# Kernel optimization log

Hardware: AMD Instinct MI355X
Metric: run time of the kernel (lower is better)

The kernel has to match this reference:

```python
import jax, jax.numpy as jnp
import numpy as np

E, C, L, B = 8, 128, 1024, 32
FB = L // 2 + 1        # 513 freq bins
HD = 2 * FB            # 1026 hidden dim


def setup_inputs() -> dict:
    key = jax.random.key(0)
    ks = jax.random.split(key, 8)
    return {
        "X_time": jax.random.normal(ks[0], (B, C, L), jnp.float32),
        "bound_params": jax.random.normal(ks[1], (E - 1,), jnp.float32),
        "W1r": jax.random.normal(ks[2], (E, HD, FB), jnp.float32) * 0.1,
        "W1i": jax.random.normal(ks[3], (E, HD, FB), jnp.float32) * 0.1,
        "b1r": jnp.zeros((E, HD), jnp.float32),
        "b1i": jnp.zeros((E, HD), jnp.float32),
        "W2r": jax.random.normal(ks[4], (E, FB, HD), jnp.float32) * 0.1,
        "W2i": jax.random.normal(ks[5], (E, FB, HD), jnp.float32) * 0.1,
        "b2r": jnp.zeros((E, FB), jnp.float32),
        "b2i": jnp.zeros((E, FB), jnp.float32),
        "gate_W": jax.random.normal(ks[6], (E, FB), jnp.float32) * 0.1,
        "gate_b": jnp.zeros((E,), jnp.float32),
    }


def reference(X_time, bound_params, W1r, W1i, b1r, b1i, W2r, W2i, b2r, b2i, gate_W, gate_b):
    Bx, Cx, Lx = X_time.shape
    fb = Lx // 2 + 1
    e = W1r.shape[0]

    Xf = jnp.fft.rfft(X_time, axis=-1)                     # [B,C,FB] complex

    # learnable frequency-band binary masks
    raw = jax.nn.sigmoid(bound_params)
    bounds = jnp.sort(jnp.concatenate([jnp.zeros(1, raw.dtype), raw, jnp.ones(1, raw.dtype)]))
    idx = (bounds * (fb - 1)).astype(jnp.int32)
    starts = idx[:e]
    ends = jnp.concatenate([idx[1:e], jnp.array([fb], jnp.int32)])
    pos = jnp.arange(fb)
    masks = ((pos[None, :] >= starts[:, None]) & (pos[None, :] < ends[:, None])).astype(X_time.dtype)  # [E,FB]

    # masked spectra per expert, split into real/imag: [E,B,C,FB]
    m = masks[:, None, None, :]
    xr = Xf.real * m
    xi = Xf.imag * m

    # expert layer 1: complex linear (W [E,HD,FB]) + complex ReLU
    hr = jnp.einsum('ehf,ebcf->ebch', W1r, xr) - jnp.einsum('ehf,ebcf->ebch', W1i, xi) + b1r[:, None, None, :]
    hi = jnp.einsum('ehf,ebcf->ebch', W1r, xi) + jnp.einsum('ehf,ebcf->ebch', W1i, xr) + b1i[:, None, None, :]
    hr = jax.nn.relu(hr)
    hi = jax.nn.relu(hi)

    # expert layer 2: complex linear (W [E,FB,HD]) -> [E,B,C,FB]
    yr = jnp.einsum('efh,ebch->ebcf', W2r, hr) - jnp.einsum('efh,ebch->ebcf', W2i, hi) + b2r[:, None, None, :]
    yi = jnp.einsum('efh,ebch->ebcf', W2r, hi) + jnp.einsum('efh,ebch->ebcf', W2i, hr) + b2i[:, None, None, :]

    # gate: mean |Xf| over channels -> linear -> softmax over experts
    mag = jnp.mean(jnp.abs(Xf), axis=1)                    # [B,FB]
    gate = jax.nn.softmax(mag @ gate_W.T + gate_b, axis=-1)  # [B,E]

    comb_r = jnp.einsum('ebcf,be->bcf', yr, gate)
    comb_i = jnp.einsum('ebcf,be->bcf', yi, gate)
    return jnp.fft.irfft(jax.lax.complex(comb_r, comb_i), n=Lx, axis=-1)
```

## Files before the change

### kernel.cpp

```cpp
#include <hip/hip_runtime.h>
#include <hip/hip_bf16.h>
#include <math.h>

typedef __hip_bfloat16 bf16;
typedef __attribute__((ext_vector_type(8))) short short8;
typedef __attribute__((ext_vector_type(4))) float f32x4;

#define FB 513
#define HD 1026
#define NN 1024
#define MR 4096
#define NE 8
#define BATCH 32

#define XINT_LD 1280
#define BIAS_LD 1056
#define FINV_LD 1088
#define HP_LD   2080
#define B1_ROWS 2176
#define KCAT    16640
#define MAG_LD  520
#define FF_ROWS 1280

__device__ __forceinline__ void gload16(const void* g, void* l) {
    __builtin_amdgcn_global_load_lds((const __attribute__((address_space(1))) void*)g,
                                     (__attribute__((address_space(3))) void*)l, 16, 0, 0);
}
__device__ __forceinline__ bf16 f2b(float v) { return __float2bfloat16(v); }
__device__ __forceinline__ unsigned short f2bu(float v) {
    bf16 b = __float2bfloat16(v);
    return *reinterpret_cast<unsigned short*>(&b);
}
__device__ __forceinline__ float bu2f(unsigned short u) {
    return __uint_as_float(((unsigned)u) << 16);
}
__device__ __forceinline__ unsigned pack2(float a, float b) {
    return (unsigned)f2bu(a) | ((unsigned)f2bu(b) << 16);
}

__device__ __forceinline__ void xcd_swizzle(int* px, int* py) {
    int gx = gridDim.x;
    int orig = blockIdx.x + gx * blockIdx.y;
    int q = (gx * gridDim.y) >> 3;
    int wg = (orig & 7) * q + (orig >> 3);
    *px = wg % gx;
    *py = wg / gx;
}

__global__ void prep_kernel(const float* __restrict__ bp, int* __restrict__ se) {
    if (threadIdx.x == 0 && blockIdx.x == 0) {
        float b[9];
        b[0] = 0.0f; b[8] = 1.0f;
        for (int i = 0; i < 7; i++) b[i + 1] = 1.0f / (1.0f + expf(-bp[i]));
        for (int i = 1; i < 9; i++) { float v = b[i]; int j = i - 1;
            while (j >= 0 && b[j] > v) { b[j + 1] = b[j]; j--; } b[j + 1] = v; }
        int idx[9];
        for (int i = 0; i < 9; i++) idx[i] = (int)(b[i] * (float)(FB - 1));
        for (int e = 0; e < NE; e++) {
            se[2 * e] = idx[e];
            se[2 * e + 1] = (e < NE - 1) ? idx[e + 1] : FB;
        }
    }
}

#define N_FF  ((long)FF_ROWS * NN)
#define N_FI  (1024L * FINV_LD)
#define N_B1P ((long)NE * B1_ROWS * (XINT_LD / 2))
#define N_XP  ((long)MR * NN / 2)
#define N_PREP (N_FF + N_FI + N_B1P + N_XP)

__global__ void prep_bulk(const float* __restrict__ W1r, const float* __restrict__ W1i,
                          const float* __restrict__ X, const int* __restrict__ se,
                          bf16* __restrict__ Ffwd, bf16* __restrict__ Finv,
                          bf16* __restrict__ B1, bf16* __restrict__ Xb) {
    long i = (long)blockIdx.x * 256 + threadIdx.x;
    const float TWO_PI = 6.283185307179586f;
    if (i < N_FF) {
        int n = (int)(i >> 10), t = (int)(i & (NN - 1));
        float v = 0.0f;
        if (n < 2 * FB) {
            int f = n >> 1, k = (f * t) & (NN - 1);
            float s, c; sincosf(TWO_PI * (float)k / (float)NN, &s, &c);
            v = (n & 1) ? -s : c;
        }
        Ffwd[i] = f2b(v);
        return;
    }
    i -= N_FF;
    if (i < N_FI) {
        int t = (int)(i / FINV_LD), k = (int)(i % FINV_LD);
        float v = 0.0f;
        if (k < 2 * FB) {
            int f = k >> 1, kk = (f * t) & (NN - 1);
            float s, c; sincosf(TWO_PI * (float)kk / (float)NN, &s, &c);
            float cf = (f == 0 || f == FB - 1) ? 1.0f : 2.0f;
            float sc = cf * (1.0f / (float)NN);
            v = (k & 1) ? -s * sc : c * sc;
        }
        Finv[i] = f2b(v);
        return;
    }
    i -= N_FI;
    if (i < N_B1P) {
        int f = (int)(i % (XINT_LD / 2));
        long t = i / (XINT_LD / 2);
        int n = (int)(t % B1_ROWS);
        int e = (int)(t / B1_ROWS);
        float ve = 0.0f, vo = 0.0f;
        if (n < 2 * HD && f < FB && f >= se[2 * e] && f < se[2 * e + 1]) {
            int hi_part = (n >= HD);
            int h = hi_part ? n - HD : n;
            long wi = ((long)e * HD + h) * FB + f;
            float wr = W1r[wi], wim = W1i[wi];
            ve = hi_part ? wim : wr;
            vo = hi_part ? wr : -wim;
        }
        *(unsigned*)(B1 + ((size_t)(e * B1_ROWS + n)) * XINT_LD + 2 * f) = pack2(ve, vo);
        return;
    }
    i -= N_B1P;
    if (i < N_XP) {
        float2 v = ((const float2*)X)[i];
        *(unsigned*)(Xb + 2 * i) = pack2(v.x, v.y);
    }
}

__global__ void pack_B2t(const float* __restrict__ W2r, const float* __restrict__ W2i,
                         bf16* __restrict__ B2t) {
    __shared__ float sR[64][65], sI[64][65];
    int e = blockIdx.z;
    int f0 = blockIdx.x * 64;
    int h0 = blockIdx.y * 64;
    int tid = threadIdx.x;
#pragma unroll
    for (int rep = 0; rep < 16; rep++) {
        int idx = tid + rep * 256;
        int fl = idx >> 6, hl = idx & 63;
        int f = f0 + fl, h = h0 + hl;
        bool ok = (f < FB) && (h < HD);
        size_t wi = ((size_t)e * FB + f) * HD + h;
        sR[fl][hl] = ok ? W2r[wi] : 0.0f;
        sI[fl][hl] = ok ? W2i[wi] : 0.0f;
    }
    __syncthreads();
#pragma unroll
    for (int rep = 0; rep < 4; rep++) {
        int idx = tid + rep * 256;
        int hl = idx >> 4, ch = idx & 15;
        int h = h0 + hl;
        int c0 = 2 * f0 + ch * 8;
        if (c0 >= FINV_LD) continue;
        short8 lo, hi;
#pragma unroll
        for (int j = 0; j < 4; j++) {
            int fl = ch * 4 + j;
            float wr = sR[fl][hl], wim = sI[fl][hl];
            lo[2 * j]     = (short)f2bu(wr);
            lo[2 * j + 1] = (short)f2bu(wim);
            hi[2 * j]     = (short)f2bu(-wim);
            hi[2 * j + 1] = (short)f2bu(wr);
        }
        if (h < HD) {
            *(short8*)(B2t + ((size_t)e * HP_LD + h) * FINV_LD + c0) = lo;
            *(short8*)(B2t + ((size_t)e * HP_LD + HD + h) * FINV_LD + c0) = hi;
        } else if (HD + h < HP_LD) {
            short8 z = {};
            *(short8*)(B2t + ((size_t)e * HP_LD + HD + h) * FINV_LD + c0) = z;
        }
    }
}

__global__ void mag_kernel(const bf16* __restrict__ Xint, float* __restrict__ magp) {
    int b = blockIdx.x, g = blockIdx.y, t = threadIdx.x;
    float acc[3] = {0.0f, 0.0f, 0.0f};
    const bf16* base = Xint + ((size_t)b * 128 + g * 16) * XINT_LD;
    for (int c = 0; c < 16; c++) {
        const bf16* row = base + (size_t)c * XINT_LD;
#pragma unroll
        for (int kk = 0; kk < 3; kk++) {
            int f = t + 256 * kk;
            if (f < FB) {
                float xr = __bfloat162float(row[2 * f]);
                float xi = __bfloat162float(row[2 * f + 1]);
                acc[kk] += sqrtf(xr * xr + xi * xi);
            }
        }
    }
#pragma unroll
    for (int kk = 0; kk < 3; kk++) {
        int f = t + 256 * kk;
        if (f < FB) magp[((size_t)b * 8 + g) * MAG_LD + f] = acc[kk];
    }
}

__global__ void gate_bias_kernel(const float* __restrict__ magp, const float* __restrict__ gW,
                                 const float* __restrict__ gb, const float* __restrict__ b2r,
                                 const float* __restrict__ b2i, float* __restrict__ gate,
                                 float* __restrict__ biasCs) {
    __shared__ float sred[256];
    __shared__ float sg[8];
    int b = blockIdx.x, tid = threadIdx.x;
    int e = tid & 7, j = tid >> 3;
    float acc = 0.0f;
    for (int f = j; f < FB; f += 32) {
        float m = 0.0f;
#pragma unroll
        for (int g = 0; g < 8; g++) m += magp[((size_t)b * 8 + g) * MAG_LD + f];
        acc += m * (1.0f / 128.0f) * gW[e * FB + f];
    }
    sred[tid] = acc;
    __syncthreads();
    if (tid < 64) {
        float a = sred[tid] + sred[tid + 64] + sred[tid + 128] + sred[tid + 192];
        a += __shfl_xor(a, 8); a += __shfl_xor(a, 16); a += __shfl_xor(a, 32);
        float logit = a + gb[e];
        float mx = logit;
        mx = fmaxf(mx, __shfl_xor(mx, 1)); mx = fmaxf(mx, __shfl_xor(mx, 2)); mx = fmaxf(mx, __shfl_xor(mx, 4));
        float ex = expf(logit - mx);
        float sum = ex;
        sum += __shfl_xor(sum, 1); sum += __shfl_xor(sum, 2); sum += __shfl_xor(sum, 4);
        if (tid < 8) { float g_ = ex / sum; sg[tid] = g_; gate[b * NE + tid] = g_; }
    }
    __syncthreads();
    for (int c = tid; c < BIAS_LD; c += 256) {
        float v = 0.0f;
        if (c < 2 * FB) {
            int f = c >> 1;
            const float* bb = (c & 1) ? b2i : b2r;
#pragma unroll
            for (int ee = 0; ee < NE; ee++) v += sg[ee] * bb[ee * FB + f];
            float cf = (f == 0 || f == FB - 1) ? 1.0f : 2.0f;
            v *= cf * (1.0f / (float)NN);
        }
        biasCs[b * BIAS_LD + c] = v;
    }
}

__global__ void biasT_kernel(const float* __restrict__ biasCs, const bf16* __restrict__ Ffwd,
                             float* __restrict__ biasT) {
    int t = blockIdx.x * 256 + threadIdx.x;
    int b = blockIdx.y;
    float s = 0.0f;
    for (int c = 0; c < 2 * FB; c++)
        s += biasCs[b * BIAS_LD + c] * __bfloat162float(Ffwd[(size_t)c * NN + t]);
    biasT[b * NN + t] = s;
}

__global__ void reduce_out4(const bf16* __restrict__ planes, const float* __restrict__ biasT,
                            float* __restrict__ out) {
    long idx = (long)blockIdx.x * 256 + threadIdx.x;
    if (idx >= (long)MR * NN / 8) return;
    size_t base = (size_t)idx * 8;
    long r = base >> 10;
    int t = (int)(base & (NN - 1));
    float s[8] = {};
#pragma unroll
    for (int z = 0; z < 4; z++) {
        short8 v = *(const short8*)(planes + (size_t)z * MR * NN + base);
#pragma unroll
        for (int j = 0; j < 8; j++) s[j] += bu2f((unsigned short)v[j]);
    }
    const float* bT = biasT + (r >> 7) * NN + t;
    float4 o0 = {s[0] + bT[0], s[1] + bT[1], s[2] + bT[2], s[3] + bT[3]};
    float4 o1 = {s[4] + bT[4], s[5] + bT[5], s[6] + bT[6], s[7] + bT[7]};
    *(float4*)(out + base) = o0;
    *(float4*)(out + base + 4) = o1;
}

template <int EPI>
__global__ void gemm_mfma(const bf16* __restrict__ A, int lda,
                          const bf16* __restrict__ B, int ldb, size_t zBstride,
                          void* __restrict__ Cv, int ldc, size_t zCoff,
                          int N, int K, int kPerZ,
                          const int* __restrict__ se2,
                          const float* __restrict__ biasR, const float* __restrict__ biasI,
                          int zBias, const float* __restrict__ gate8) {
    __shared__ bf16 As[128 * 32];
    __shared__ bf16 Bs[128 * 32];
    int tid = threadIdx.x;
    int zz = blockIdx.z;
    int bx, by;
    xcd_swizzle(&bx, &by);
    int row0 = by * 128, col0 = bx * 128;
    const bf16* Bz = B + (size_t)zz * zBstride;

    int kS, kE;
    if (EPI == 1) { int s = se2[2 * zz], e = se2[2 * zz + 1]; kS = (2 * s) & ~31; kE = (2 * e + 31) & ~31; }
    else          { kS = zz * kPerZ; kE = min(K, kS + kPerZ); }

    f32x4 acc[4][4] = {};

    int lane = tid & 63, wid = tid >> 6;
    int wrB = (wid >> 1) << 6, wcB = (wid & 1) << 6;
    int lr = lane & 15, lk = (lane >> 4) << 3;

    int r_a = tid >> 2, c_a = (tid & 3) << 3;
    int r_b = (tid + 256) >> 2, c_b = ((tid + 256) & 3) << 3;

    for (int kt = kS; kt < kE; kt += 32) {
        gload16(A + (size_t)(row0 + r_a) * lda + kt + c_a, &As[(size_t)tid * 8]);
        gload16(A + (size_t)(row0 + r_b) * lda + kt + c_b, &As[((size_t)tid + 256) * 8]);
        gload16(Bz + (size_t)(col0 + r_a) * ldb + kt + c_a, &Bs[(size_t)tid * 8]);
        gload16(Bz + (size_t)(col0 + r_b) * ldb + kt + c_b, &Bs[((size_t)tid + 256) * 8]);
        __syncthreads();
        short8 av[4], bv[4];
#pragma unroll
        for (int m = 0; m < 4; m++)
            av[m] = *(const short8*)&As[(wrB + m * 16 + lr) * 32 + lk];
#pragma unroll
        for (int n = 0; n < 4; n++)
            bv[n] = *(const short8*)&Bs[(wcB + n * 16 + lr) * 32 + lk];
#pragma unroll
        for (int m = 0; m < 4; m++)
#pragma unroll
            for (int n = 0; n < 4; n++)
                acc[m][n] = __builtin_amdgcn_mfma_f32_16x16x32_bf16(av[m], bv[n], acc[m][n], 0, 0, 0);
        __syncthreads();
    }

    int r0 = row0 + wrB + ((lane >> 4) << 2);
    int c0i = col0 + wcB + (lane & 15);
    float g = (EPI == 1) ? gate8[(row0 >> 7) * NE + zz] : 0.0f;

#pragma unroll
    for (int m = 0; m < 4; m++)
#pragma unroll
        for (int n = 0; n < 4; n++) {
            int c = c0i + n * 16;
            if (c >= N) continue;
#pragma unroll
            for (int j = 0; j < 4; j++) {
                int r = r0 + m * 16 + j;
                float v = acc[m][n][j];
                if (EPI == 1) {
                    v += (c < HD) ? biasR[zz * zBias + c] : biasI[zz * zBias + c - HD];
                    v = fmaxf(v, 0.0f) * g;
                    ((bf16*)Cv + (size_t)zz * zCoff)[(size_t)r * ldc + c] = f2b(v);
                } else {
                    ((float*)Cv + (size_t)zz * zCoff)[(size_t)r * ldc + c] = v;
                }
            }
        }
}

__device__ __forceinline__ void stage_half(const bf16* gbase, int ld, int kt,
                                           bf16* ldsBase, int tid) {
#pragma unroll
    for (int j = 0; j < 2; j++) {
        int r = j * 64 + (tid >> 3);
        int sc = ((tid & 7) ^ ((tid >> 3) & 7)) * 8;
        gload16(gbase + (size_t)r * ld + kt + sc, ldsBase + j * 4096 + tid * 8);
    }
}

#define MF(a, b, c) __builtin_amdgcn_mfma_f32_16x16x32_bf16(a, b, c, 0, 0, 0)
#define RD(off) (*(const short8*)(bc + (off)))
#define LOADA(dst, FM)                                                        \
    dst[0] = RD(aBase + (FM) * 1024 + cb0);                                   \
    dst[1] = RD(aBase + (FM) * 1024 + cb1);                                   \
    dst[2] = RD(aBase + (FM + 1) * 1024 + cb0);                               \
    dst[3] = RD(aBase + (FM + 1) * 1024 + cb1);
#define CLUST(FM, av)                                                         \
    __builtin_amdgcn_s_setprio(1);                                            \
    acc[FM][0] = MF(av[0], b0[0], acc[FM][0]);                                \
    acc[FM][0] = MF(av[1], b1[0], acc[FM][0]);                                \
    acc[FM][1] = MF(av[0], b0[1], acc[FM][1]);                                \
    acc[FM][1] = MF(av[1], b1[1], acc[FM][1]);                                \
    acc[FM][2] = MF(av[0], b0[2], acc[FM][2]);                                \
    acc[FM][2] = MF(av[1], b1[2], acc[FM][2]);                                \
    acc[FM][3] = MF(av[0], b0[3], acc[FM][3]);                                \
    acc[FM][3] = MF(av[1], b1[3], acc[FM][3]);                                \
    acc[FM + 1][0] = MF(av[2], b0[0], acc[FM + 1][0]);                        \
    acc[FM + 1][0] = MF(av[3], b1[0], acc[FM + 1][0]);                        \
    acc[FM + 1][1] = MF(av[2], b0[1], acc[FM + 1][1]);                        \
    acc[FM + 1][1] = MF(av[3], b1[1], acc[FM + 1][1]);                        \
    acc[FM + 1][2] = MF(av[2], b0[2], acc[FM + 1][2]);                        \
    acc[FM + 1][2] = MF(av[3], b1[2], acc[FM + 1][2]);                        \
    acc[FM + 1][3] = MF(av[2], b0[3], acc[FM + 1][3]);                        \
    acc[FM + 1][3] = MF(av[3], b1[3], acc[FM + 1][3]);                        \
    __builtin_amdgcn_s_setprio(0);
#define PBAR { __builtin_amdgcn_sched_barrier(0); __builtin_amdgcn_s_barrier(); }

__device__ __forceinline__ void gemm8p_body(
        bf16* sm, const bf16* __restrict__ A, int lda,
        const bf16* __restrict__ B, int ldb,
        bf16* __restrict__ C, int ldc,
        int row0, int col0, int kS, int nt) {
    int tid = threadIdx.x;
    const bf16* Ab = A + (size_t)row0 * lda;
    const bf16* Bb = B + (size_t)col0 * ldb;

    stage_half(Ab, lda, kS, sm, tid);
    stage_half(Ab + (size_t)128 * lda, lda, kS, sm + 8192, tid);
    stage_half(Bb, ldb, kS, sm + 16384, tid);
    stage_half(Bb + (size_t)128 * ldb, ldb, kS, sm + 24576, tid);

    f32x4 acc[8][4] = {};

    int l = tid & 63, w = tid >> 6;
    int wm = w >> 2, wn = w & 3;
    int lr = l & 15, lk4 = l >> 4;
    int swz = lr & 7;
    int cb0 = ((lk4) ^ swz) * 8;
    int cb1 = ((4 + lk4) ^ swz) * 8;
    int aBase = wm * 8192 + lr * 64;
    int bBase = 16384 + (wn >> 1) * 8192 + (wn & 1) * 4096 + lr * 64;

    for (int t = 0; t < nt; ++t) {
        const int cur = t & 1;
        const bf16* bc = sm + cur * 32768;
        bf16* bufN = sm + (cur ^ 1) * 32768;
        int ktn = kS + (t + 1) * 64;
        bool more = (t + 1) < nt;
        if (more) {
            stage_half(Ab, lda, ktn, bufN, tid);
            stage_half(Ab + (size_t)128 * lda, lda, ktn, bufN + 8192, tid);
            asm volatile("s_waitcnt vmcnt(4)" ::: "memory");
        } else {
            asm volatile("s_waitcnt vmcnt(0)" ::: "memory");
        }
        __builtin_amdgcn_s_barrier();
        __builtin_amdgcn_sched_barrier(0);
        short8 b0[4], b1[4], a0[4], a1[4], a2[4], a3[4];
#pragma unroll
        for (int n = 0; n < 4; n++) {
            b0[n] = RD(bBase + n * 1024 + cb0);
            b1[n] = RD(bBase + n * 1024 + cb1);
        }
        LOADA(a0, 0)
        LOADA(a1, 2)
        __builtin_amdgcn_sched_barrier(0);
        CLUST(0, a0)
        if (more) {
            stage_half(Bb, ldb, ktn, bufN + 16384, tid);
            stage_half(Bb + (size_t)128 * ldb, ldb, ktn, bufN + 24576, tid);
        }
        LOADA(a2, 4)
        PBAR
        CLUST(2, a1)
        LOADA(a3, 6)
        PBAR
        CLUST(4, a2)
        PBAR
        CLUST(6, a3)
        PBAR
    }

    int rb = row0 + wm * 128 + lk4 * 4;
    int cbase = col0 + wn * 64 + lr;
#pragma unroll
    for (int fm = 0; fm < 8; fm++)
#pragma unroll
        for (int n = 0; n < 4; n++)
#pragma unroll
            for (int j = 0; j < 4; j++)
                C[(size_t)(rb + fm * 16 + j) * ldc + cbase + n * 16] = f2b(acc[fm][n][j]);
}

__global__ __launch_bounds__(512, 2) void gemm8p_combo(
        const bf16* A0, int lda0, const bf16* B0, int ldb0, bf16* C0, int ldc0,
        int gx0, int nt0, int nb0,
        const bf16* A1, int lda1, const bf16* B1w, int ldb1, bf16* C1, int ldc1,
        int gx1, int nt1) {
    __shared__ bf16 sm[65536];
    int id = blockIdx.x;
    bool p0 = id < nb0;
    const bf16* A = p0 ? A0 : A1; int lda = p0 ? lda0 : lda1;
    const bf16* B = p0 ? B0 : B1w; int ldb = p0 ? ldb0 : ldb1;
    bf16* C = p0 ? C0 : C1; int ldc = p0 ? ldc0 : ldc1;
    int gx = p0 ? gx0 : gx1, nt = p0 ? nt0 : nt1;
    int id2 = p0 ? id : id - nb0;
    int bx = id2 % gx, by = id2 / gx;
    gemm8p_body(sm, A, lda, B, ldb, C, ldc, by * 256, bx * 256, 0, nt);
}

__global__ __launch_bounds__(512, 2) void gemm8p_l2(
        const bf16* __restrict__ A, int lda, const bf16* __restrict__ B, int ldb,
        bf16* __restrict__ C, int ldc, size_t zCoff, int tilesPerZ) {
    __shared__ bf16 sm[65536];
    int id = blockIdx.x;
    int by_z = (id & 7) * 8 + (id >> 5);
    int bx = (id >> 3) & 3;
    int z = by_z >> 4;
    int by = by_z & 15;
    gemm8p_body(sm, A, lda, B, ldb, C + (size_t)z * zCoff, ldc,
                by * 256, bx * 256, z * tilesPerZ * 64, tilesPerZ);
}

extern "C" void kernel_launch(void* const* d_in, const int* in_sizes, int n_in,
                              void* d_out, int out_size, void* d_ws, size_t ws_size,
                              hipStream_t stream) {
    const float* X   = (const float*)d_in[0];
    const float* bp  = (const float*)d_in[1];
    const float* W1r = (const float*)d_in[2];
    const float* W1i = (const float*)d_in[3];
    const float* b1r = (const float*)d_in[4];
    const float* b1i = (const float*)d_in[5];
    const float* W2r = (const float*)d_in[6];
    const float* W2i = (const float*)d_in[7];
    const float* b2r = (const float*)d_in[8];
    const float* b2i = (const float*)d_in[9];
    const float* gW  = (const float*)d_in[10];
    const float* gb  = (const float*)d_in[11];
    float* out = (float*)d_out;

    const size_t SZH = (size_t)MR * HP_LD * 2;

    char* p = (char*)d_ws;
    auto alloc = [&](size_t bytes) -> char* {
        char* r = p; p += (bytes + 255) & ~255ULL; return r;
    };
    int*   se     = (int*)alloc(64 * 4);
    float* magp   = (float*)alloc((size_t)BATCH * 8 * MAG_LD * 4);
    float* gate   = (float*)alloc((size_t)BATCH * NE * 4);
    float* biasCs = (float*)alloc((size_t)BATCH * BIAS_LD * 4);
    float* biasT  = (float*)alloc((size_t)BATCH * NN * 4);
    bf16*  Ffwd   = (bf16*)alloc((size_t)FF_ROWS * NN * 2);
    bf16*  Finv   = (bf16*)alloc((size_t)NN * FINV_LD * 2);
    char*  b1slot = alloc((size_t)NE * B1_ROWS * XINT_LD * 2);
    bf16*  B1     = (bf16*)b1slot;
    bf16*  planesB = (bf16*)b1slot;
    bf16*  B2t    = (bf16*)alloc((size_t)KCAT * FINV_LD * 2);
    bf16*  Xint   = (bf16*)alloc((size_t)MR * XINT_LD * 2);
    bf16*  B2inv  = (bf16*)alloc((size_t)NN * KCAT * 2);
    bf16*  Hp     = (bf16*)alloc(8 * SZH);
    bf16*  Xb     = (bf16*)((char*)Hp + 8 * SZH - (size_t)MR * NN * 2);

    prep_kernel<<<1, 64, 0, stream>>>(bp, se);
    prep_bulk<<<(unsigned)((N_PREP + 255) / 256), 256, 0, stream>>>(
        W1r, W1i, X, se, Ffwd, Finv, B1, Xb);
    pack_B2t<<<dim3(9, 17, 8), 256, 0, stream>>>(W2r, W2i, B2t);

    gemm8p_combo<<<340, 512, 0, stream>>>(
        Finv, FINV_LD, B2t, FINV_LD, B2inv, KCAT, 65, 17, 260,
        Xb, NN, Ffwd, NN, Xint, XINT_LD, 5, 16);

    mag_kernel<<<dim3(BATCH, 8), 256, 0, stream>>>(Xint, magp);
    gate_bias_kernel<<<BATCH, 256, 0, stream>>>(magp, gW, gb, b2r, b2i, gate, biasCs);
    biasT_kernel<<<dim3(4, BATCH), 256, 0, stream>>>(biasCs, Ffwd, biasT);

    gemm_mfma<1><<<dim3(17, 32, 8), 256, 0, stream>>>(
        Xint, XINT_LD, B1, XINT_LD, (size_t)B1_ROWS * XINT_LD,
        Hp, KCAT, HP_LD, 2 * HD, 0, 0,
        se, b1r, b1i, HD, gate);

    gemm8p_l2<<<256, 512, 0, stream>>>(
        Hp, KCAT, B2inv, KCAT, planesB, NN, (size_t)MR * NN, 65);

    reduce_out4<<<(unsigned)(((size_t)MR * NN / 8 + 255) / 256), 256, 0, stream>>>(
        planesB, biasT, out);
}
```

Measured before the change: 379.8 us.

## Switch 8-wave GEMM to 32x32 MFMA and fuse prep and bias kernels

The main 8-wave GEMM body moves from 16x16x32 bf16 MFMA to 32x32x16 bf16 MFMA, with new LDS read offsets and a new accumulator layout and store pattern. The aim is fewer LDS reads and MFMA issues per tile. Separately, pack_B2t is merged into the bulk prep kernel and biasT_kernel into gate_bias_kernel, which removes two launches. The cost is that the fused bias matvec now runs on only 32 blocks, and the larger accumulators may raise register pressure.

```diff
diff --git a/kernel.cpp b/kernel.cpp
--- a/kernel.cpp
+++ b/kernel.cpp
@@ -5,6 +5,7 @@
 typedef __hip_bfloat16 bf16;
 typedef __attribute__((ext_vector_type(8))) short short8;
 typedef __attribute__((ext_vector_type(4))) float f32x4;
+typedef __attribute__((ext_vector_type(16))) float f32x16;
 
 #define FB 513
 #define HD 1026
@@ -14,7 +15,6 @@
 #define BATCH 32
 
 #define XINT_LD 1280
-#define BIAS_LD 1056
 #define FINV_LD 1088
 #define HP_LD   2080
 #define B1_ROWS 2176
@@ -68,12 +68,62 @@
 #define N_B1P ((long)NE * B1_ROWS * (XINT_LD / 2))
 #define N_XP  ((long)MR * NN / 2)
 #define N_PREP (N_FF + N_FI + N_B1P + N_XP)
-
-__global__ void prep_bulk(const float* __restrict__ W1r, const float* __restrict__ W1i,
-                          const float* __restrict__ X, const int* __restrict__ se,
-                          bf16* __restrict__ Ffwd, bf16* __restrict__ Finv,
-                          bf16* __restrict__ B1, bf16* __restrict__ Xb) {
-    long i = (long)blockIdx.x * 256 + threadIdx.x;
+#define NB_BULK 61184
+#define NB_B2T  1224
+
+__global__ void prep_all(const float* __restrict__ W1r, const float* __restrict__ W1i,
+                         const float* __restrict__ W2r, const float* __restrict__ W2i,
+                         const float* __restrict__ X, const int* __restrict__ se,
+                         bf16* __restrict__ Ffwd, bf16* __restrict__ Finv,
+                         bf16* __restrict__ B1, bf16* __restrict__ B2t,
+                         bf16* __restrict__ Xb) {
+    __shared__ float sR[64][65], sI[64][65];
+    int tid = threadIdx.x;
+    if (blockIdx.x >= NB_BULK) {
+        int bid2 = blockIdx.x - NB_BULK;
+        int fx = bid2 % 9;
+        int hy = (bid2 / 9) % 17;
+        int e = bid2 / 153;
+        int f0 = fx * 64, h0 = hy * 64;
+#pragma unroll
+        for (int rep = 0; rep < 16; rep++) {
+            int idx = tid + rep * 256;
+            int fl = idx >> 6, hl = idx & 63;
+            int f = f0 + fl, h = h0 + hl;
+            bool ok = (f < FB) && (h < HD);
+            size_t wi = ((size_t)e * FB + f) * HD + h;
+            sR[fl][hl] = ok ? W2r[wi] : 0.0f;
+            sI[fl][hl] = ok ? W2i[wi] : 0.0f;
+        }
+        __syncthreads();
+#pragma unroll
+        for (int rep = 0; rep < 4; rep++) {
+            int idx = tid + rep * 256;
+            int hl = idx >> 4, ch = idx & 15;
+            int h = h0 + hl;
+            int c0 = 2 * f0 + ch * 8;
+            if (c0 >= FINV_LD) continue;
+            short8 lo, hi;
+#pragma unroll
+            for (int j = 0; j < 4; j++) {
+                int fl = ch * 4 + j;
+                float wr = sR[fl][hl], wim = sI[fl][hl];
+                lo[2 * j]     = (short)f2bu(wr);
+                lo[2 * j + 1] = (short)f2bu(wim);
+                hi[2 * j]     = (short)f2bu(-wim);
+                hi[2 * j + 1] = (short)f2bu(wr);
+            }
+            if (h < HD) {
+                *(short8*)(B2t + ((size_t)e * HP_LD + h) * FINV_LD + c0) = lo;
+                *(short8*)(B2t + ((size_t)e * HP_LD + HD + h) * FINV_LD + c0) = hi;
+            } else if (HD + h < HP_LD) {
+                short8 z = {};
+                *(short8*)(B2t + ((size_t)e * HP_LD + HD + h) * FINV_LD + c0) = z;
+            }
+        }
+        return;
+    }
+    long i = (long)blockIdx.x * 256 + tid;
     const float TWO_PI = 6.283185307179586f;
     if (i < N_FF) {
         int n = (int)(i >> 10), t = (int)(i & (NN - 1));
@@ -125,51 +175,6 @@
     }
 }
 
-__global__ void pack_B2t(const float* __restrict__ W2r, const float* __restrict__ W2i,
-                         bf16* __restrict__ B2t) {
-    __shared__ float sR[64][65], sI[64][65];
-    int e = blockIdx.z;
-    int f0 = blockIdx.x * 64;
-    int h0 = blockIdx.y * 64;
-    int tid = threadIdx.x;
-#pragma unroll
-    for (int rep = 0; rep < 16; rep++) {
-        int idx = tid + rep * 256;
-        int fl = idx >> 6, hl = idx & 63;
-        int f = f0 + fl, h = h0 + hl;
-        bool ok = (f < FB) && (h < HD);
-        size_t wi = ((size_t)e * FB + f) * HD + h;
-        sR[fl][hl] = ok ? W2r[wi] : 0.0f;
-        sI[fl][hl] = ok ? W2i[wi] : 0.0f;
-    }
-    __syncthreads();
-#pragma unroll
-    for (int rep = 0; rep < 4; rep++) {
-        int idx = tid + rep * 256;
-        int hl = idx >> 4, ch = idx & 15;
-        int h = h0 + hl;
-        int c0 = 2 * f0 + ch * 8;
-        if (c0 >= FINV_LD) continue;
-        short8 lo, hi;
-#pragma unroll
-        for (int j = 0; j < 4; j++) {
-            int fl = ch * 4 + j;
-            float wr = sR[fl][hl], wim = sI[fl][hl];
-            lo[2 * j]     = (short)f2bu(wr);
-            lo[2 * j + 1] = (short)f2bu(wim);
-            hi[2 * j]     = (short)f2bu(-wim);
-            hi[2 * j + 1] = (short)f2bu(wr);
-        }
-        if (h < HD) {
-            *(short8*)(B2t + ((size_t)e * HP_LD + h) * FINV_LD + c0) = lo;
-            *(short8*)(B2t + ((size_t)e * HP_LD + HD + h) * FINV_LD + c0) = hi;
-        } else if (HD + h < HP_LD) {
-            short8 z = {};
-            *(short8*)(B2t + ((size_t)e * HP_LD + HD + h) * FINV_LD + c0) = z;
-        }
-    }
-}
-
 __global__ void mag_kernel(const bf16* __restrict__ Xint, float* __restrict__ magp) {
     int b = blockIdx.x, g = blockIdx.y, t = threadIdx.x;
     float acc[3] = {0.0f, 0.0f, 0.0f};
@@ -195,10 +200,11 @@
 
 __global__ void gate_bias_kernel(const float* __restrict__ magp, const float* __restrict__ gW,
                                  const float* __restrict__ gb, const float* __restrict__ b2r,
-                                 const float* __restrict__ b2i, float* __restrict__ gate,
-                                 float* __restrict__ biasCs) {
+                                 const float* __restrict__ b2i, const bf16* __restrict__ Ffwd,
+                                 float* __restrict__ gate, float* __restrict__ biasT) {
     __shared__ float sred[256];
     __shared__ float sg[8];
+    __shared__ float sbias[2 * FB];
     int b = blockIdx.x, tid = threadIdx.x;
     int e = tid & 7, j = tid >> 3;
     float acc = 0.0f;
@@ -222,28 +228,22 @@
         if (tid < 8) { float g_ = ex / sum; sg[tid] = g_; gate[b * NE + tid] = g_; }
     }
     __syncthreads();
-    for (int c = tid; c < BIAS_LD; c += 256) {
+    for (int c = tid; c < 2 * FB; c += 256) {
+        int f = c >> 1;
+        const float* bb = (c & 1) ? b2i : b2r;
         float v = 0.0f;
-        if (c < 2 * FB) {
-            int f = c >> 1;
-            const float* bb = (c & 1) ? b2i : b2r;
-#pragma unroll
-            for (int ee = 0; ee < NE; ee++) v += sg[ee] * bb[ee * FB + f];
-            float cf = (f == 0 || f == FB - 1) ? 1.0f : 2.0f;
-            v *= cf * (1.0f / (float)NN);
-        }
-        biasCs[b * BIAS_LD + c] = v;
-    }
-}
-
-__global__ void biasT_kernel(const float* __restrict__ biasCs, const bf16* __restrict__ Ffwd,
-                             float* __restrict__ biasT) {
-    int t = blockIdx.x * 256 + threadIdx.x;
-    int b = blockIdx.y;
-    float s = 0.0f;
-    for (int c = 0; c < 2 * FB; c++)
-        s += biasCs[b * BIAS_LD + c] * __bfloat162float(Ffwd[(size_t)c * NN + t]);
-    biasT[b * NN + t] = s;
+#pragma unroll
+        for (int ee = 0; ee < NE; ee++) v += sg[ee] * bb[ee * FB + f];
+        float cf = (f == 0 || f == FB - 1) ? 1.0f : 2.0f;
+        sbias[c] = v * cf * (1.0f / (float)NN);
+    }
+    __syncthreads();
+    for (int t = tid; t < NN; t += 256) {
+        float s = 0.0f;
+        for (int c = 0; c < 2 * FB; c++)
+            s += sbias[c] * __bfloat162float(Ffwd[(size_t)c * NN + t]);
+        biasT[b * NN + t] = s;
+    }
 }
 
 __global__ void reduce_out4(const bf16* __restrict__ planes, const float* __restrict__ biasT,
@@ -353,31 +353,23 @@
     }
 }
 
-#define MF(a, b, c) __builtin_amdgcn_mfma_f32_16x16x32_bf16(a, b, c, 0, 0, 0)
+#define MF32(a, b, c) __builtin_amdgcn_mfma_f32_32x32x16_bf16(a, b, c, 0, 0, 0)
 #define RD(off) (*(const short8*)(bc + (off)))
-#define LOADA(dst, FM)                                                        \
-    dst[0] = RD(aBase + (FM) * 1024 + cb0);                                   \
-    dst[1] = RD(aBase + (FM) * 1024 + cb1);                                   \
-    dst[2] = RD(aBase + (FM + 1) * 1024 + cb0);                               \
-    dst[3] = RD(aBase + (FM + 1) * 1024 + cb1);
-#define CLUST(FM, av)                                                         \
+#define LOADA32(dst, RM)                                                      \
+    dst[0] = RD(aBase + (RM) * 2048 + cs0);                                   \
+    dst[1] = RD(aBase + (RM) * 2048 + cs1);                                   \
+    dst[2] = RD(aBase + (RM) * 2048 + cs2);                                   \
+    dst[3] = RD(aBase + (RM) * 2048 + cs3);
+#define CLUST32(RM, av)                                                       \
     __builtin_amdgcn_s_setprio(1);                                            \
-    acc[FM][0] = MF(av[0], b0[0], acc[FM][0]);                                \
-    acc[FM][0] = MF(av[1], b1[0], acc[FM][0]);                                \
-    acc[FM][1] = MF(av[0], b0[1], acc[FM][1]);                                \
-    acc[FM][1] = MF(av[1], b1[1], acc[FM][1]);                                \
-    acc[FM][2] = MF(av[0], b0[2], acc[FM][2]);                                \
-    acc[FM][2] = MF(av[1], b1[2], acc[FM][2]);                                \
-    acc[FM][3] = MF(av[0], b0[3], acc[FM][3]);                                \
-    acc[FM][3] = MF(av[1], b1[3], acc[FM][3]);                                \
-    acc[FM + 1][0] = MF(av[2], b0[0], acc[FM + 1][0]);                        \
-    acc[FM + 1][0] = MF(av[3], b1[0], acc[FM + 1][0]);                        \
-    acc[FM + 1][1] = MF(av[2], b0[1], acc[FM + 1][1]);                        \
-    acc[FM + 1][1] = MF(av[3], b1[1], acc[FM + 1][1]);                        \
-    acc[FM + 1][2] = MF(av[2], b0[2], acc[FM + 1][2]);                        \
-    acc[FM + 1][2] = MF(av[3], b1[2], acc[FM + 1][2]);                        \
-    acc[FM + 1][3] = MF(av[2], b0[3], acc[FM + 1][3]);                        \
-    acc[FM + 1][3] = MF(av[3], b1[3], acc[FM + 1][3]);                        \
+    acc[RM][0] = MF32(av[0], b0[0], acc[RM][0]);                              \
+    acc[RM][1] = MF32(av[0], b1[0], acc[RM][1]);                              \
+    acc[RM][0] = MF32(av[1], b0[1], acc[RM][0]);                              \
+    acc[RM][1] = MF32(av[1], b1[1], acc[RM][1]);                              \
+    acc[RM][0] = MF32(av[2], b0[2], acc[RM][0]);                              \
+    acc[RM][1] = MF32(av[2], b1[2], acc[RM][1]);                              \
+    acc[RM][0] = MF32(av[3], b0[3], acc[RM][0]);                              \
+    acc[RM][1] = MF32(av[3], b1[3], acc[RM][1]);                              \
     __builtin_amdgcn_s_setprio(0);
 #define PBAR { __builtin_amdgcn_sched_barrier(0); __builtin_amdgcn_s_barrier(); }
 
@@ -395,16 +387,18 @@
     stage_half(Bb, ldb, kS, sm + 16384, tid);
     stage_half(Bb + (size_t)128 * ldb, ldb, kS, sm + 24576, tid);
 
-    f32x4 acc[8][4] = {};
+    f32x16 acc[4][2] = {};
 
     int l = tid & 63, w = tid >> 6;
     int wm = w >> 2, wn = w & 3;
-    int lr = l & 15, lk4 = l >> 4;
-    int swz = lr & 7;
-    int cb0 = ((lk4) ^ swz) * 8;
-    int cb1 = ((4 + lk4) ^ swz) * 8;
-    int aBase = wm * 8192 + lr * 64;
-    int bBase = 16384 + (wn >> 1) * 8192 + (wn & 1) * 4096 + lr * 64;
+    int lr32 = l & 31, lk2 = l >> 5;
+    int swz = lr32 & 7;
+    int cs0 = ((0 + lk2) ^ swz) * 8;
+    int cs1 = ((2 + lk2) ^ swz) * 8;
+    int cs2 = ((4 + lk2) ^ swz) * 8;
+    int cs3 = ((6 + lk2) ^ swz) * 8;
+    int aBase = wm * 8192 + lr32 * 64;
+    int bBase = 16384 + wn * 4096 + lr32 * 64;
 
     for (int t = 0; t < nt; ++t) {
         const int cur = t & 1;
@@ -422,39 +416,42 @@
         __builtin_amdgcn_s_barrier();
         __builtin_amdgcn_sched_barrier(0);
         short8 b0[4], b1[4], a0[4], a1[4], a2[4], a3[4];
-#pragma unroll
-        for (int n = 0; n < 4; n++) {
-            b0[n] = RD(bBase + n * 1024 + cb0);
-            b1[n] = RD(bBase + n * 1024 + cb1);
-        }
-        LOADA(a0, 0)
-        LOADA(a1, 2)
+        b0[0] = RD(bBase + cs0); b1[0] = RD(bBase + 2048 + cs0);
+        b0[1] = RD(bBase + cs1); b1[1] = RD(bBase + 2048 + cs1);
+        b0[2] = RD(bBase + cs2); b1[2] = RD(bBase + 2048 + cs2);
+        b0[3] = RD(bBase + cs3); b1[3] = RD(bBase + 2048 + cs3);
+        LOADA32(a0, 0)
+        LOADA32(a1, 1)
         __builtin_amdgcn_sched_barrier(0);
-        CLUST(0, a0)
+        CLUST32(0, a0)
         if (more) {
             stage_half(Bb, ldb, ktn, bufN + 16384, tid);
             stage_half(Bb + (size_t)128 * ldb, ldb, ktn, bufN + 24576, tid);
         }
-        LOADA(a2, 4)
+        LOADA32(a2, 2)
         PBAR
-        CLUST(2, a1)
-        LOADA(a3, 6)
+        CLUST32(1, a1)
+        LOADA32(a3, 3)
         PBAR
-        CLUST(4, a2)
+        CLUST32(2, a2)
         PBAR
-        CLUST(6, a3)
+        CLUST32(3, a3)
         PBAR
     }
 
-    int rb = row0 + wm * 128 + lk4 * 4;
-    int cbase = col0 + wn * 64 + lr;
-#pragma unroll
-    for (int fm = 0; fm < 8; fm++)
-#pragma unroll
-        for (int n = 0; n < 4; n++)
-#pragma unroll
-            for (int j = 0; j < 4; j++)
-                C[(size_t)(rb + fm * 16 + j) * ldc + cbase + n * 16] = f2b(acc[fm][n][j]);
+    int colE = col0 + wn * 64 + lr32;
+    int rbase = row0 + wm * 128 + 4 * lk2;
+#pragma unroll
+    for (int rm = 0; rm < 4; rm++)
+#pragma unroll
+        for (int cn = 0; cn < 2; cn++) {
+            f32x16 v = acc[rm][cn];
+#pragma unroll
+            for (int reg = 0; reg < 16; reg++) {
+                int r = rbase + rm * 32 + (reg & 3) + 8 * (reg >> 2);
+                C[(size_t)r * ldc + colE + cn * 32] = f2b(v[reg]);
+            }
+        }
 }
 
 __global__ __launch_bounds__(512, 2) void gemm8p_combo(
@@ -513,7 +510,6 @@
     int*   se     = (int*)alloc(64 * 4);
     float* magp   = (float*)alloc((size_t)BATCH * 8 * MAG_LD * 4);
     float* gate   = (float*)alloc((size_t)BATCH * NE * 4);
-    float* biasCs = (float*)alloc((size_t)BATCH * BIAS_LD * 4);
     float* biasT  = (float*)alloc((size_t)BATCH * NN * 4);
     bf16*  Ffwd   = (bf16*)alloc((size_t)FF_ROWS * NN * 2);
     bf16*  Finv   = (bf16*)alloc((size_t)NN * FINV_LD * 2);
@@ -527,17 +523,16 @@
     bf16*  Xb     = (bf16*)((char*)Hp + 8 * SZH - (size_t)MR * NN * 2);
 
     prep_kernel<<<1, 64, 0, stream>>>(bp, se);
-    prep_bulk<<<(unsigned)((N_PREP + 255) / 256), 256, 0, stream>>>(
-        W1r, W1i, X, se, Ffwd, Finv, B1, Xb);
-    pack_B2t<<<dim3(9, 17, 8), 256, 0, stream>>>(W2r, W2i, B2t);
+    prep_all<<<NB_BULK + NB_B2T, 256, 0, stream>>>(
+        W1r, W1i, W2r, W2i, X, se, Ffwd, Finv, B1, B2t, Xb);
 
     gemm8p_combo<<<340, 512, 0, stream>>>(
         Finv, FINV_LD, B2t, FINV_LD, B2inv, KCAT, 65, 17, 260,
         Xb, NN, Ffwd, NN, Xint, XINT_LD, 5, 16);
 
     mag_kernel<<<dim3(BATCH, 8), 256, 0, stream>>>(Xint, magp);
-    gate_bias_kernel<<<BATCH, 256, 0, stream>>>(magp, gW, gb, b2r, b2i, gate, biasCs);
-    biasT_kernel<<<dim3(4, BATCH), 256, 0, stream>>>(biasCs, Ffwd, biasT);
+    gate_bias_kernel<<<BATCH, 256, 0, stream>>>(magp, gW, gb, b2r, b2i, Ffwd,
+                                                gate, biasT);
 
     gemm_mfma<1><<<dim3(17, 32, 8), 256, 0, stream>>>(
         Xint, XINT_LD, B1, XINT_LD, (size_t)B1_ROWS * XINT_LD,
```

After: 533.5 us. 40.5% more time.
